# Kernel tuning notes

Hardware: AMD Instinct MI355X
Metric: run time of the kernel (lower is better)

## Reference

```python
import jax, jax.numpy as jnp
import numpy as np

B, S, OUT = 256, 256, 64
IN = 4 * S * S


def setup_inputs() -> dict:
    key = jax.random.key(0)
    k1, k2, k3 = jax.random.split(key, 3)
    x = jax.random.normal(k1, (B, IN), dtype=jnp.float32)
    # nn.Linear init scale ~ 1/sqrt(fan_in); exact distribution irrelevant for correctness
    W = jax.random.normal(k2, (OUT, IN), dtype=jnp.float32) * (1.0 / np.sqrt(IN))
    b = jax.random.normal(k3, (OUT,), dtype=jnp.float32) * (1.0 / np.sqrt(IN))
    return {"x": x, "W": W, "b": b}


def _haar_dwt2_features(x):
    # x: [B, 4*S*S] viewed as [B, 4, S, S]; single-level Haar dwt2 per channel.
    # pywt haar: approx=(e+o)/sqrt2, detail=(e-o)/sqrt2 along each axis =>
    # with 2x2 block [[a,b],[c,d]]: LL=(a+b+c+d)/2, cH=(a+b-c-d)/2,
    # cV=(a-b+c-d)/2, cD=(a-b-c+d)/2; code concatenates [LL, cH, cV, cD]
    # per channel, then channels.
    Bn = x.shape[0]
    s = int(np.sqrt(x.shape[1] // 4))
    x4 = x.reshape(Bn, 4, s, s)
    a = x4[:, :, 0::2, 0::2]
    bq = x4[:, :, 0::2, 1::2]
    c = x4[:, :, 1::2, 0::2]
    d = x4[:, :, 1::2, 1::2]
    LL = (a + bq + c + d) * 0.5
    LH = (a + bq - c - d) * 0.5  # pywt cH
    HL = (a - bq + c - d) * 0.5  # pywt cV
    HH = (a - bq - c + d) * 0.5  # pywt cD
    # [B, 4ch, 4subband, s/2, s/2] -> flatten: channel-major, subband next
    t = jnp.stack([LL, LH, HL, HH], axis=2)
    return t.reshape(Bn, -1)


def reference(x, W, b):
    t = _haar_dwt2_features(x)
    # original wraps transform in torch.no_grad()
    t = jax.lax.stop_gradient(t)
    return t @ W.T + b
```

## Files before the change

kernel.cpp:

```cpp
#include <hip/hip_runtime.h>
#include <hip/hip_bf16.h>
#include <stdint.h>


#define IN_K 262144
#define HS   128
#define LDA  72

typedef short bf16x8 __attribute__((ext_vector_type(8)));
typedef float f32x4  __attribute__((ext_vector_type(4)));

__device__ __forceinline__ uint32_t pack2_bf16(float a, float b) {
    uint32_t ua = __float_as_uint(a);
    uint32_t ub = __float_as_uint(b);
    ua = (ua + 0x7fffu + ((ua >> 16) & 1u)) >> 16;
    ub = (ub + 0x7fffu + ((ub >> 16) & 1u)) >> 16;
    return ua | (ub << 16);
}

__global__ __launch_bounds__(512) void wavelet_gemm(
    const float* __restrict__ x, const float* __restrict__ W,
    float* __restrict__ part)
{
    __shared__ short Ash[256 * LDA];
    __shared__ short Bsh[64 * LDA];

    const int tid  = threadIdx.x;
    const int lane = tid & 63;
    const int wave = tid >> 6;
    const int l16  = lane & 15;
    const int l4   = lane >> 4;
    const int wm   = wave * 32;

    f32x4 acc[2][4];
#pragma unroll
    for (int mi = 0; mi < 2; mi++)
#pragma unroll
        for (int ni = 0; ni < 4; ni++)
            acc[mi][ni] = (f32x4){0.f, 0.f, 0.f, 0.f};

    for (int s = blockIdx.x; s < 4096; s += gridDim.x) {
        const int ci = s >> 3;
        const int jg = s & 7;
        const int c  = ci >> 7;
        const int i  = ci & 127;

        const int row0 = (c * 256 + 2 * i) * 256 + 32 * jg;
#pragma unroll
        for (int p = tid; p < 2048; p += 512) {
            const int b   = p >> 3;
            const int jj4 = p & 7;
            const float4 f0 = *(const float4*)(x + (size_t)b * IN_K + row0 + jj4 * 4);
            const float4 f1 = *(const float4*)(x + (size_t)b * IN_K + row0 + 256 + jj4 * 4);
            const float s1a = f0.x + f0.y, s2a = f1.x + f1.y;
            const float d1a = f0.x - f0.y, d2a = f1.x - f1.y;
            const float s1b = f0.z + f0.w, s2b = f1.z + f1.w;
            const float d1b = f0.z - f0.w, d2b = f1.z - f1.w;
            const int jl = jj4 * 2;
            short* arow = &Ash[b * LDA + jl];
            *(uint32_t*)(arow +  0) = pack2_bf16(s1a + s2a, s1b + s2b);
            *(uint32_t*)(arow + 16) = pack2_bf16(s1a - s2a, s1b - s2b);
            *(uint32_t*)(arow + 32) = pack2_bf16(d1a + d2a, d1b + d2b);
            *(uint32_t*)(arow + 48) = pack2_bf16(d1a - d2a, d1b - d2b);
        }

#pragma unroll
        for (int v = tid; v < 1024; v += 512) {
            const int o   = v >> 4;
            const int q   = (v >> 2) & 3;
            const int jj4 = v & 3;
            const float4 f = *(const float4*)(W + (size_t)o * IN_K
                                + (c * 4 + q) * 16384 + i * 128 + 16 * jg + jj4 * 4);
            short* brow = &Bsh[o * LDA + q * 16 + jj4 * 4];
            *(uint32_t*)(brow + 0) = pack2_bf16(f.x, f.y);
            *(uint32_t*)(brow + 2) = pack2_bf16(f.z, f.w);
        }

        __syncthreads();

#pragma unroll
        for (int kh = 0; kh < 2; kh++) {
            const int ko = kh * 32 + l4 * 8;
            bf16x8 a0 = *(const bf16x8*)&Ash[(wm + l16) * LDA + ko];
            bf16x8 a1 = *(const bf16x8*)&Ash[(wm + 16 + l16) * LDA + ko];
#pragma unroll
            for (int ni = 0; ni < 4; ni++) {
                bf16x8 bf = *(const bf16x8*)&Bsh[(ni * 16 + l16) * LDA + ko];
                acc[0][ni] = __builtin_amdgcn_mfma_f32_16x16x32_bf16(a0, bf, acc[0][ni], 0, 0, 0);
                acc[1][ni] = __builtin_amdgcn_mfma_f32_16x16x32_bf16(a1, bf, acc[1][ni], 0, 0, 0);
            }
        }

        __syncthreads();
    }

    float* p = part + (size_t)blockIdx.x * (256 * 64);
#pragma unroll
    for (int mi = 0; mi < 2; mi++)
#pragma unroll
        for (int ni = 0; ni < 4; ni++)
#pragma unroll
            for (int r = 0; r < 4; r++) {
                const int m = wm + mi * 16 + l4 * 4 + r;
                const int n = ni * 16 + l16;
                p[m * 64 + n] = acc[mi][ni][r];
            }
}

__global__ __launch_bounds__(256) void wavelet_reduce(
    const float* __restrict__ part, const float* __restrict__ bias,
    float* __restrict__ out, int nblk)
{
    __shared__ float red[4][64];
    const int e_l = threadIdx.x & 63;
    const int g   = threadIdx.x >> 6;
    const int e0  = blockIdx.x * 64;
    float acc = 0.f;
    for (int blk = g; blk < nblk; blk += 4)
        acc += part[(size_t)blk * 16384 + e0 + e_l];
    red[g][e_l] = acc;
    __syncthreads();
    if (g == 0) {
        const float v = red[0][e_l] + red[1][e_l] + red[2][e_l] + red[3][e_l];
        out[e0 + e_l] = 0.5f * v + bias[e_l];
    }
}

extern "C" void kernel_launch(void* const* d_in, const int* in_sizes, int n_in,
                              void* d_out, int out_size, void* d_ws, size_t ws_size,
                              hipStream_t stream)
{
    const float* x = (const float*)d_in[0];
    const float* W = (const float*)d_in[1];
    const float* b = (const float*)d_in[2];
    float* out  = (float*)d_out;
    float* part = (float*)d_ws;

    int nb = (int)(ws_size / (size_t)(16384 * 4));
    if (nb > 512) nb = 512;
    if (nb < 1)  nb = 1;

    wavelet_gemm<<<nb, 512, 0, stream>>>(x, W, part);
    wavelet_reduce<<<256, 256, 0, stream>>>(part, b, out, nb);
}
```

Baseline: 445.6 us.

## Load MFMA fragments directly from global memory, dropping LDS staging and barriers

The GEMM no longer stages the Haar-transformed x tile and the W tile through shared memory. Each lane now loads the exact elements of its MFMA A and B fragments straight from global memory, computing the Haar combinations in registers and reordering K inside each fragment consistently for both operands. This removes the LDS writes, LDS reads and both __syncthreads per iteration. In exchange, W is reloaded redundantly by all 8 waves and the global accesses become narrower (float2 for W) and more scattered, which can raise L2 traffic. The reduce loop also gets an unroll hint.

Measured after the change: 530.3 us. 1.19x slower.

```diff
diff --git a/kernel.cpp b/kernel.cpp
--- a/kernel.cpp
+++ b/kernel.cpp
@@ -4,8 +4,6 @@
 
 
 #define IN_K 262144
-#define HS   128
-#define LDA  72
 
 typedef short bf16x8 __attribute__((ext_vector_type(8)));
 typedef float f32x4  __attribute__((ext_vector_type(4)));
@@ -22,9 +20,6 @@
     const float* __restrict__ x, const float* __restrict__ W,
     float* __restrict__ part)
 {
-    __shared__ short Ash[256 * LDA];
-    __shared__ short Bsh[64 * LDA];
-
     const int tid  = threadIdx.x;
     const int lane = tid & 63;
     const int wave = tid >> 6;
@@ -45,53 +40,59 @@
         const int c  = ci >> 7;
         const int i  = ci & 127;
 
-        const int row0 = (c * 256 + 2 * i) * 256 + 32 * jg;
+        const int xoff = c * 65536 + 2 * i * 256 + 32 * jg + 4 * l4;
+        const int woff = c * 65536 + i * 128 + 16 * jg + 2 * l4;
+
+        bf16x8 bfrag[2][4];
 #pragma unroll
-        for (int p = tid; p < 2048; p += 512) {
-            const int b   = p >> 3;
-            const int jj4 = p & 7;
-            const float4 f0 = *(const float4*)(x + (size_t)b * IN_K + row0 + jj4 * 4);
-            const float4 f1 = *(const float4*)(x + (size_t)b * IN_K + row0 + 256 + jj4 * 4);
-            const float s1a = f0.x + f0.y, s2a = f1.x + f1.y;
-            const float d1a = f0.x - f0.y, d2a = f1.x - f1.y;
-            const float s1b = f0.z + f0.w, s2b = f1.z + f1.w;
-            const float d1b = f0.z - f0.w, d2b = f1.z - f1.w;
-            const int jl = jj4 * 2;
-            short* arow = &Ash[b * LDA + jl];
-            *(uint32_t*)(arow +  0) = pack2_bf16(s1a + s2a, s1b + s2b);
-            *(uint32_t*)(arow + 16) = pack2_bf16(s1a - s2a, s1b - s2b);
-            *(uint32_t*)(arow + 32) = pack2_bf16(d1a + d2a, d1b + d2b);
-            *(uint32_t*)(arow + 48) = pack2_bf16(d1a - d2a, d1b - d2b);
+        for (int kh = 0; kh < 2; kh++) {
+#pragma unroll
+            for (int ni = 0; ni < 4; ni++) {
+                const float* wp = W + (size_t)(ni * 16 + l16) * IN_K
+                                    + woff + 8 * kh;
+                const float2 v0 = *(const float2*)(wp);
+                const float2 v1 = *(const float2*)(wp + 16384);
+                const float2 v2 = *(const float2*)(wp + 32768);
+                const float2 v3 = *(const float2*)(wp + 49152);
+                union { bf16x8 v; uint32_t u[4]; } bu;
+                bu.u[0] = pack2_bf16(v0.x, v1.x);
+                bu.u[1] = pack2_bf16(v2.x, v3.x);
+                bu.u[2] = pack2_bf16(v0.y, v1.y);
+                bu.u[3] = pack2_bf16(v2.y, v3.y);
+                bfrag[kh][ni] = bu.v;
+            }
+        }
+
+        bf16x8 afrag[2][2];
+#pragma unroll
+        for (int mi = 0; mi < 2; mi++) {
+            const float* xp = x + (size_t)(wm + mi * 16 + l16) * IN_K + xoff;
+#pragma unroll
+            for (int kh = 0; kh < 2; kh++) {
+                const float4 f0 = *(const float4*)(xp + 16 * kh);
+                const float4 f1 = *(const float4*)(xp + 16 * kh + 256);
+                const float s1 = f0.x + f0.y, d1 = f0.x - f0.y;
+                const float s2 = f1.x + f1.y, d2 = f1.x - f1.y;
+                const float t1 = f0.z + f0.w, e1 = f0.z - f0.w;
+                const float t2 = f1.z + f1.w, e2 = f1.z - f1.w;
+                union { bf16x8 v; uint32_t u[4]; } au;
+                au.u[0] = pack2_bf16(s1 + s2, s1 - s2);
+                au.u[1] = pack2_bf16(d1 + d2, d1 - d2);
+                au.u[2] = pack2_bf16(t1 + t2, t1 - t2);
+                au.u[3] = pack2_bf16(e1 + e2, e1 - e2);
+                afrag[mi][kh] = au.v;
+            }
         }
 
 #pragma unroll
-        for (int v = tid; v < 1024; v += 512) {
-            const int o   = v >> 4;
-            const int q   = (v >> 2) & 3;
-            const int jj4 = v & 3;
-            const float4 f = *(const float4*)(W + (size_t)o * IN_K
-                                + (c * 4 + q) * 16384 + i * 128 + 16 * jg + jj4 * 4);
-            short* brow = &Bsh[o * LDA + q * 16 + jj4 * 4];
-            *(uint32_t*)(brow + 0) = pack2_bf16(f.x, f.y);
-            *(uint32_t*)(brow + 2) = pack2_bf16(f.z, f.w);
-        }
-
-        __syncthreads();
-
-#pragma unroll
-        for (int kh = 0; kh < 2; kh++) {
-            const int ko = kh * 32 + l4 * 8;
-            bf16x8 a0 = *(const bf16x8*)&Ash[(wm + l16) * LDA + ko];
-            bf16x8 a1 = *(const bf16x8*)&Ash[(wm + 16 + l16) * LDA + ko];
+        for (int kh = 0; kh < 2; kh++)
 #pragma unroll
             for (int ni = 0; ni < 4; ni++) {
-                bf16x8 bf = *(const bf16x8*)&Bsh[(ni * 16 + l16) * LDA + ko];
-                acc[0][ni] = __builtin_amdgcn_mfma_f32_16x16x32_bf16(a0, bf, acc[0][ni], 0, 0, 0);
-                acc[1][ni] = __builtin_amdgcn_mfma_f32_16x16x32_bf16(a1, bf, acc[1][ni], 0, 0, 0);
+                acc[0][ni] = __builtin_amdgcn_mfma_f32_16x16x32_bf16(
+                    afrag[0][kh], bfrag[kh][ni], acc[0][ni], 0, 0, 0);
+                acc[1][ni] = __builtin_amdgcn_mfma_f32_16x16x32_bf16(
+                    afrag[1][kh], bfrag[kh][ni], acc[1][ni], 0, 0, 0);
             }
-        }
-
-        __syncthreads();
     }
 
     float* p = part + (size_t)blockIdx.x * (256 * 64);
@@ -116,6 +117,7 @@
     const int g   = threadIdx.x >> 6;
     const int e0  = blockIdx.x * 64;
     float acc = 0.f;
+#pragma unroll 8
     for (int blk = g; blk < nblk; blk += 4)
         acc += part[(size_t)blk * 16384 + e0 + e_l];
     red[g][e_l] = acc;
```
